# Kernel tuning notes

Measured on AMD Instinct MI355X. Metric: run time of the kernel, lower is better.

The kernel has to match this reference:

```python
import jax, jax.numpy as jnp
import numpy as np

NEG_SLOPE = 0.2

def gat_conv(x, src, dst, W, a_src, a_dst, bias, N):
    # PyG GATConv, heads=1: h = xW; e_ij = LeakyReLU(a_src.h_j + a_dst.h_i)
    h = x @ W                                   # [N, H]
    as_ = h @ a_src                             # [N]
    ad_ = h @ a_dst                             # [N]
    e = jax.nn.leaky_relu(as_[src] + ad_[dst], NEG_SLOPE)   # [E]
    m = jax.ops.segment_max(e, dst, num_segments=N)          # per-target max
    w = jnp.exp(e - m[dst])
    denom = jax.ops.segment_sum(w, dst, num_segments=N)
    alpha = w / (denom[dst] + 1e-16)                          # [E]
    out = jax.ops.segment_sum(alpha[:, None] * h[src], dst, num_segments=N)
    return out + bias


def setup_inputs() -> dict:
    key = jax.random.key(0)
    N, E, D, H, A = 20000, 320000, 256, 256, 8
    ks = jax.random.split(key, 16)
    s = lambda k, shp, fan: jax.random.normal(k, shp, jnp.float32) * (1.0 / np.sqrt(fan))
    return {
        "obs": jax.random.normal(ks[0], (N, D), jnp.float32),
        "edge_index": jax.random.randint(ks[1], (2, E), 0, N, dtype=jnp.int32),
        "W1": s(ks[2], (D, H), D), "a1_src": s(ks[3], (H,), H), "a1_dst": s(ks[4], (H,), H), "b1": jnp.zeros((H,), jnp.float32),
        "W2": s(ks[5], (H, H), H), "a2_src": s(ks[6], (H,), H), "a2_dst": s(ks[7], (H,), H), "b2": jnp.zeros((H,), jnp.float32),
        "Wm1": s(ks[8], (H, H), H), "bm1": jnp.zeros((H,), jnp.float32),
        "Wm2": s(ks[9], (H, A), H), "bm2": jnp.zeros((A,), jnp.float32),
    }


def reference(obs, edge_index, W1, a1_src, a1_dst, b1, W2, a2_src, a2_dst, b2, Wm1, bm1, Wm2, bm2):
    N = obs.shape[0]
    loops = jnp.arange(N, dtype=edge_index.dtype)
    src = jnp.concatenate([edge_index[0], loops])   # add self-loops (PyG default)
    dst = jnp.concatenate([edge_index[1], loops])
    x = jax.nn.relu(gat_conv(obs, src, dst, W1, a1_src, a1_dst, b1, N))
    x = jax.nn.relu(gat_conv(x,   src, dst, W2, a2_src, a2_dst, b2, N))
    x = jax.nn.relu(x @ Wm1 + bm1)
    return jnp.tanh(x @ Wm2 + bm2)
```

## Files before the change

### kernel.cpp

```cpp
#include <hip/hip_runtime.h>
#include <hip/hip_bf16.h>
#include <math.h>
#include <stdio.h>

typedef __attribute__((ext_vector_type(8))) short short8;
typedef __attribute__((ext_vector_type(4))) float f32x4;
typedef __attribute__((ext_vector_type(4))) unsigned short us4;

__device__ __forceinline__ float us2f(unsigned short u) {
    return __uint_as_float(((unsigned)u) << 16);
}
__device__ __forceinline__ unsigned short f2us_rtn(float f) {
    return (unsigned short)__bfloat16_as_ushort(__float2bfloat16(f));
}

__device__ __forceinline__ void stage8(const unsigned short* Ap, unsigned short* dst) {
    *(short8*)dst = *(const short8*)Ap;
}
__device__ __forceinline__ void stage8(const float* Ap, unsigned short* dst) {
    const float4 a = *(const float4*)Ap;
    const float4 b = *(const float4*)(Ap + 4);
    const float f[8] = {a.x, a.y, a.z, a.w, b.x, b.y, b.z, b.w};
    short8 o;
#pragma unroll
    for (int e = 0; e < 8; e++) o[e] = (short)f2us_rtn(f[e]);
    *(short8*)dst = o;
}

__global__ void prep_all(const float* __restrict__ Wa, const float* __restrict__ Wb,
                         const float* __restrict__ Wc,
                         unsigned short* __restrict__ TA, unsigned short* __restrict__ TB,
                         unsigned short* __restrict__ TC,
                         float* __restrict__ as1, float* __restrict__ ad1,
                         float* __restrict__ as2, float* __restrict__ ad2,
                         int* __restrict__ deg,
                         int K, int Nn, int N) {
    const int tot = K * Nn;
    int idx = blockIdx.x * blockDim.x + threadIdx.x;
    if (idx < 3 * tot) {
        const float* W;
        unsigned short* T;
        if (idx < tot) { W = Wa; T = TA; }
        else if (idx < 2 * tot) { W = Wb; T = TB; idx -= tot; }
        else { W = Wc; T = TC; idx -= 2 * tot; }
        const int n = idx / K, k = idx - n * K;
        T[idx] = f2us_rtn(W[(size_t)k * Nn + n]);
        return;
    }
    idx -= 3 * tot;
    if (idx < 5 * N) {
        if (idx < N) as1[idx] = 0.f;
        else if (idx < 2 * N) ad1[idx - N] = 0.f;
        else if (idx < 3 * N) as2[idx - 2 * N] = 0.f;
        else if (idx < 4 * N) ad2[idx - 3 * N] = 0.f;
        else deg[idx - 4 * N] = 0;
    }
}

#define LP 72
template <typename TA>
__global__ __launch_bounds__(256) void gemm_mfma(const TA* __restrict__ A,
                                                 const unsigned short* __restrict__ Bt,
                                                 const float* __restrict__ avs,
                                                 const float* __restrict__ avd,
                                                 float* __restrict__ as_,
                                                 float* __restrict__ ad_,
                                                 unsigned short* __restrict__ C,
                                                 int M, int Nn, int K) {
    __shared__ unsigned short sA[64 * LP];
    __shared__ unsigned short sB[128 * LP];
    const int tid = threadIdx.x;
    const int wave = tid >> 6, lane = tid & 63;
    const int m16 = lane & 15, quad = lane >> 4;
    const int row0 = blockIdx.x * 64, col0 = blockIdx.y * 128;
    const int wr = (wave >> 1) * 32, wc = (wave & 1) * 64;
    const int ar = tid >> 2, akc = (tid & 3) * 8;
    const int bkc = (tid & 7) * 8, bcb = tid >> 3;

    f32x4 acc[2][4] = {};
    for (int k0 = 0; k0 < K; k0 += 64) {
        {
            const int gr = (row0 + ar) < M ? (row0 + ar) : (M - 1);
            const TA* Ap = A + (size_t)gr * K + k0 + akc;
            stage8(Ap,      &sA[ar * LP + akc]);
            stage8(Ap + 32, &sA[ar * LP + akc + 32]);
        }
#pragma unroll
        for (int q = 0; q < 4; q++) {
            const int colq = bcb + 32 * q;
            *(short8*)&sB[colq * LP + bkc] =
                *(const short8*)(Bt + (size_t)(col0 + colq) * K + k0 + bkc);
        }
        __syncthreads();
#pragma unroll
        for (int ks = 0; ks < 2; ks++) {
            short8 ah[2];
#pragma unroll
            for (int mi = 0; mi < 2; mi++)
                ah[mi] = *(const short8*)&sA[(wr + mi * 16 + m16) * LP + ks * 32 + quad * 8];
#pragma unroll
            for (int ni = 0; ni < 4; ni++) {
                const short8 bv = *(const short8*)&sB[(wc + ni * 16 + m16) * LP + ks * 32 + quad * 8];
#pragma unroll
                for (int mi = 0; mi < 2; mi++)
                    acc[mi][ni] = __builtin_amdgcn_mfma_f32_16x16x32_bf16(ah[mi], bv, acc[mi][ni], 0, 0, 0);
            }
        }
        __syncthreads();
    }
    float ps[2][4] = {}, pd[2][4] = {};
#pragma unroll
    for (int mi = 0; mi < 2; mi++) {
        const int orow_base = row0 + wr + mi * 16 + quad * 4;
#pragma unroll
        for (int ni = 0; ni < 4; ni++) {
            const int ocol = col0 + wc + ni * 16 + m16;
            const float asv = avs[ocol], adv = avd[ocol];
#pragma unroll
            for (int r = 0; r < 4; r++) {
                const int orow = orow_base + r;
                if (orow < M) {
                    const float v = acc[mi][ni][r];
                    C[(size_t)orow * Nn + ocol] = f2us_rtn(v);
                    ps[mi][r] = fmaf(v, asv, ps[mi][r]);
                    pd[mi][r] = fmaf(v, adv, pd[mi][r]);
                }
            }
        }
    }
#pragma unroll
    for (int mi = 0; mi < 2; mi++)
#pragma unroll
        for (int r = 0; r < 4; r++)
#pragma unroll
            for (int off = 1; off < 16; off <<= 1) {
                ps[mi][r] += __shfl_xor(ps[mi][r], off);
                pd[mi][r] += __shfl_xor(pd[mi][r], off);
            }
    if (m16 == 0) {
#pragma unroll
        for (int mi = 0; mi < 2; mi++) {
            const int orow_base = row0 + wr + mi * 16 + quad * 4;
#pragma unroll
            for (int r = 0; r < 4; r++) {
                const int orow = orow_base + r;
                if (orow < M) {
                    atomicAdd(&as_[orow], ps[mi][r]);
                    atomicAdd(&ad_[orow], pd[mi][r]);
                }
            }
        }
    }
}

__global__ __launch_bounds__(256) void gemm_head(const unsigned short* __restrict__ A,
                                                 const unsigned short* __restrict__ Bt,
                                                 const float* __restrict__ bias1,
                                                 const float* __restrict__ W2,
                                                 const float* __restrict__ bias2,
                                                 float* __restrict__ out,
                                                 int M, int K, int Aout) {
    __shared__ unsigned short sA[64 * LP];
    __shared__ unsigned short sB[256 * LP];
    __shared__ float pLDS[2][64][8];
    const int tid = threadIdx.x;
    const int wave = tid >> 6, lane = tid & 63;
    const int m16 = lane & 15, quad = lane >> 4;
    const int row0 = blockIdx.x * 64;
    const int wr = (wave >> 1) * 32, wc = (wave & 1) * 128;
    const int ar = tid >> 2, akc = (tid & 3) * 8;
    const int bkc = (tid & 7) * 8, bcb = tid >> 3;

    f32x4 acc[2][8] = {};
    for (int k0 = 0; k0 < K; k0 += 64) {
        {
            const int gr = (row0 + ar) < M ? (row0 + ar) : (M - 1);
            const unsigned short* Ap = A + (size_t)gr * K + k0 + akc;
            *(short8*)&sA[ar * LP + akc]      = *(const short8*)Ap;
            *(short8*)&sA[ar * LP + akc + 32] = *(const short8*)(Ap + 32);
        }
#pragma unroll
        for (int q = 0; q < 8; q++) {
            const int colq = bcb + 32 * q;
            *(short8*)&sB[colq * LP + bkc] =
                *(const short8*)(Bt + (size_t)colq * K + k0 + bkc);
        }
        __syncthreads();
#pragma unroll
        for (int ks = 0; ks < 2; ks++) {
            short8 ah[2];
#pragma unroll
            for (int mi = 0; mi < 2; mi++)
                ah[mi] = *(const short8*)&sA[(wr + mi * 16 + m16) * LP + ks * 32 + quad * 8];
#pragma unroll
            for (int ni = 0; ni < 8; ni++) {
                const short8 bv = *(const short8*)&sB[(wc + ni * 16 + m16) * LP + ks * 32 + quad * 8];
#pragma unroll
                for (int mi = 0; mi < 2; mi++)
                    acc[mi][ni] = __builtin_amdgcn_mfma_f32_16x16x32_bf16(ah[mi], bv, acc[mi][ni], 0, 0, 0);
            }
        }
        __syncthreads();
    }
    float p[2][4][8] = {};
#pragma unroll
    for (int ni = 0; ni < 8; ni++) {
        const int ocol = wc + ni * 16 + m16;
        const float b1v = bias1[ocol];
        float w2[8];
#pragma unroll
        for (int a = 0; a < 8; a++) w2[a] = W2[ocol * 8 + a];
#pragma unroll
        for (int mi = 0; mi < 2; mi++)
#pragma unroll
            for (int r = 0; r < 4; r++) {
                const float v = fmaxf(acc[mi][ni][r] + b1v, 0.f);
#pragma unroll
                for (int a = 0; a < 8; a++) p[mi][r][a] = fmaf(v, w2[a], p[mi][r][a]);
            }
    }
#pragma unroll
    for (int off = 1; off < 16; off <<= 1)
#pragma unroll
        for (int mi = 0; mi < 2; mi++)
#pragma unroll
            for (int r = 0; r < 4; r++)
#pragma unroll
                for (int a = 0; a < 8; a++) p[mi][r][a] += __shfl_xor(p[mi][r][a], off);
    if (m16 == 0) {
        const int half = wc >> 7;
#pragma unroll
        for (int mi = 0; mi < 2; mi++) {
            const int lrow = wr + mi * 16 + quad * 4;
#pragma unroll
            for (int r = 0; r < 4; r++)
#pragma unroll
                for (int a = 0; a < 8; a++) pLDS[half][lrow + r][a] = p[mi][r][a];
        }
    }
    __syncthreads();
#pragma unroll
    for (int u = 0; u < 2; u++) {
        const int idx = tid * 2 + u;
        const int lrow = idx >> 3, a = idx & 7;
        const int orow = row0 + lrow;
        if (orow < M && a < Aout)
            out[(size_t)orow * Aout + a] =
                tanhf(pLDS[0][lrow][a] + pLDS[1][lrow][a] + bias2[a]);
    }
}
#undef LP

__global__ void count_kernel(const int* __restrict__ dstA, int* __restrict__ deg, int E, int Etot) {
    const int e = blockIdx.x * blockDim.x + threadIdx.x;
    if (e >= Etot) return;
    const int d = (e < E) ? dstA[e] : (e - E);
    atomicAdd(&deg[d], 1);
}

__global__ __launch_bounds__(1024) void scan_kernel(const int* __restrict__ deg,
                                                    int* __restrict__ offs,
                                                    int* __restrict__ cursor, int N) {
    __shared__ int sums[1024];
    const int t = threadIdx.x;
    const int chunk = (N + 1023) / 1024;
    const int start = t * chunk;
    int s = 0;
    for (int i = 0; i < chunk; i++) {
        const int p = start + i;
        if (p < N) s += deg[p];
    }
    sums[t] = s;
    __syncthreads();
    for (int off = 1; off < 1024; off <<= 1) {
        const int add = (t >= off) ? sums[t - off] : 0;
        __syncthreads();
        sums[t] += add;
        __syncthreads();
    }
    int run = (t > 0) ? sums[t - 1] : 0;
    for (int i = 0; i < chunk; i++) {
        const int p = start + i;
        if (p < N) { offs[p] = run; cursor[p] = run; run += deg[p]; }
    }
    if (t == 0) offs[N] = sums[1023];
}

__global__ void scatter_kernel(const int* __restrict__ srcA, const int* __restrict__ dstA,
                               int* __restrict__ cursor, int* __restrict__ esrc, int E, int Etot) {
    const int e = blockIdx.x * blockDim.x + threadIdx.x;
    if (e >= Etot) return;
    int s, d;
    if (e < E) { s = srcA[e]; d = dstA[e]; } else { s = d = e - E; }
    const int slot = atomicAdd(&cursor[d], 1);
    esrc[slot] = s;
}

__global__ __launch_bounds__(256) void agg_kernel(const unsigned short* __restrict__ hb,
                                                  const int* __restrict__ offs,
                                                  const int* __restrict__ esrc,
                                                  const float* __restrict__ as_,
                                                  const float* __restrict__ ad_,
                                                  const float* __restrict__ bias,
                                                  unsigned short* __restrict__ xout, int N) {
    const int n = __builtin_amdgcn_readfirstlane(blockIdx.x * 4 + (threadIdx.x >> 6));
    if (n >= N) return;
    const int lane = threadIdx.x & 63;
    const int f0 = lane * 4;
    const int b = offs[n], e2 = offs[n + 1];
    const float adn = ad_[n];
    float a0 = 0.f, a1 = 0.f, a2 = 0.f, a3 = 0.f, wsum = 0.f;
    for (int c0 = b; c0 < e2; c0 += 16) {
        int s = 0;
        float w = 0.f;
        if (lane < 16) {
            const int j = c0 + lane;
            const int jj = j < e2 ? j : e2 - 1;
            s = esrc[jj];
            if (j < e2) {
                float v = as_[s] + adn;
                v = v > 0.f ? v : 0.2f * v;
                w = __expf(v);
                wsum += w;
            }
        }
        int sb[16];
        float wb[16];
#pragma unroll
        for (int u = 0; u < 16; u++) {
            sb[u] = __shfl(s, u);
            wb[u] = __shfl(w, u);
        }
        us4 pv[16];
#pragma unroll
        for (int u = 0; u < 16; u++)
            pv[u] = *(const us4*)(hb + (unsigned)((sb[u] << 8) + f0));
#pragma unroll
        for (int u = 0; u < 16; u++) {
            a0 = fmaf(wb[u], us2f(pv[u][0]), a0);
            a1 = fmaf(wb[u], us2f(pv[u][1]), a1);
            a2 = fmaf(wb[u], us2f(pv[u][2]), a2);
            a3 = fmaf(wb[u], us2f(pv[u][3]), a3);
        }
    }
#pragma unroll
    for (int off = 32; off; off >>= 1) wsum += __shfl_xor(wsum, off);
    const float inv = 1.0f / (wsum + 1e-16f);
    us4 o;
    o[0] = f2us_rtn(fmaxf(a0 * inv + bias[f0], 0.f));
    o[1] = f2us_rtn(fmaxf(a1 * inv + bias[f0 + 1], 0.f));
    o[2] = f2us_rtn(fmaxf(a2 * inv + bias[f0 + 2], 0.f));
    o[3] = f2us_rtn(fmaxf(a3 * inv + bias[f0 + 3], 0.f));
    *(us4*)(xout + (unsigned)((n << 8) + f0)) = o;
}

extern "C" void kernel_launch(void* const* d_in, const int* in_sizes, int n_in,
                              void* d_out, int out_size, void* d_ws, size_t ws_size,
                              hipStream_t stream) {
    const float* obs = (const float*)d_in[0];
    const int* eidx  = (const int*)d_in[1];
    const float* W1  = (const float*)d_in[2];
    const float* a1s = (const float*)d_in[3];
    const float* a1d = (const float*)d_in[4];
    const float* b1  = (const float*)d_in[5];
    const float* W2  = (const float*)d_in[6];
    const float* a2s = (const float*)d_in[7];
    const float* a2d = (const float*)d_in[8];
    const float* b2v = (const float*)d_in[9];
    const float* Wm1 = (const float*)d_in[10];
    const float* bm1 = (const float*)d_in[11];
    const float* Wm2 = (const float*)d_in[12];
    const float* bm2 = (const float*)d_in[13];
    float* out = (float*)d_out;

    const int Hh = in_sizes[3];
    const int Dd = in_sizes[2] / Hh;
    const int N  = in_sizes[0] / Dd;
    const int E  = in_sizes[1] / 2;
    const int Etot = E + N;
    const int Aout = in_sizes[12] / Hh;

    const int* srcA = eidx;
    const int* dstA = eidx + E;

    size_t off = 0;
    char* ws = (char*)d_ws;
    auto alloc = [&](size_t bytes) -> char* {
        char* p = ws + off;
        off = (off + bytes + 15) & ~(size_t)15;
        return p;
    };
    unsigned short* h  = (unsigned short*)alloc((size_t)N * Hh * 2);
    unsigned short* xb = (unsigned short*)alloc((size_t)N * Hh * 2);
    float* as1   = (float*)alloc((size_t)N * 4);
    float* ad1   = (float*)alloc((size_t)N * 4);
    float* as2   = (float*)alloc((size_t)N * 4);
    float* ad2   = (float*)alloc((size_t)N * 4);
    int* deg     = (int*)alloc((size_t)N * 4);
    int* offs    = (int*)alloc((size_t)(N + 1) * 4);
    int* cursor  = (int*)alloc((size_t)N * 4);
    int* esrc    = (int*)alloc((size_t)Etot * 4);
    const size_t wsz = (size_t)Dd * Hh;
    unsigned short* W1t = (unsigned short*)alloc(wsz * 2);
    unsigned short* W2t = (unsigned short*)alloc(wsz * 2);
    unsigned short* Wmt = (unsigned short*)alloc(wsz * 2);

    const int eb = 256;
    const int eg = (Etot + eb - 1) / eb;
    const dim3 ggrid((N + 63) / 64, Hh / 128);
    const int nrow = (N + 63) / 64;
    const int nb4 = (N + 3) / 4;

    const int ptot = 3 * (int)wsz + 5 * N;
    prep_all<<<(ptot + 255) / 256, 256, 0, stream>>>(
        W1, W2, Wm1, W1t, W2t, Wmt, as1, ad1, as2, ad2, deg, Dd, Hh, N);

    count_kernel<<<eg, eb, 0, stream>>>(dstA, deg, E, Etot);
    scan_kernel<<<1, 1024, 0, stream>>>(deg, offs, cursor, N);
    scatter_kernel<<<eg, eb, 0, stream>>>(srcA, dstA, cursor, esrc, E, Etot);

    gemm_mfma<float><<<ggrid, 256, 0, stream>>>(obs, W1t, a1s, a1d, as1, ad1, h, N, Hh, Dd);
    agg_kernel<<<nb4, 256, 0, stream>>>(h, offs, esrc, as1, ad1, b1, xb, N);

    gemm_mfma<unsigned short><<<ggrid, 256, 0, stream>>>(xb, W2t, a2s, a2d, as2, ad2, h, N, Hh, Hh);
    agg_kernel<<<nb4, 256, 0, stream>>>(h, offs, esrc, as2, ad2, b2v, xb, N);

    gemm_head<<<nrow, 256, 0, stream>>>(xb, Wmt, bm1, Wm2, bm2, out, N, Hh, Aout);
}
```

Measured before the change: 265.6 us.

## Prefetch GEMM tiles into registers, pre-convert obs to bf16, widen aggregation loads

Both GEMM kernels now load the next K-tile from global memory into registers while MFMAs run on the current LDS tile, then store it to LDS after a barrier. This is meant to hide global load latency behind compute. The fp32 obs input is converted to bf16 once inside prep_all, so the first GEMM reads bf16 like the second, at the cost of an extra full pass over obs. The aggregation kernel has each half-wave handle alternate edges with 8-wide bf16 loads and combines the two halves with a cross-lane shuffle, halving the gather instructions per edge but adding a reduction step.

```diff
diff --git a/kernel.cpp b/kernel.cpp
--- a/kernel.cpp
+++ b/kernel.cpp
@@ -6,6 +6,7 @@
 typedef __attribute__((ext_vector_type(8))) short short8;
 typedef __attribute__((ext_vector_type(4))) float f32x4;
 typedef __attribute__((ext_vector_type(4))) unsigned short us4;
+typedef __attribute__((ext_vector_type(8))) unsigned short us8;
 
 __device__ __forceinline__ float us2f(unsigned short u) {
     return __uint_as_float(((unsigned)u) << 16);
@@ -14,27 +15,14 @@
     return (unsigned short)__bfloat16_as_ushort(__float2bfloat16(f));
 }
 
-__device__ __forceinline__ void stage8(const unsigned short* Ap, unsigned short* dst) {
-    *(short8*)dst = *(const short8*)Ap;
-}
-__device__ __forceinline__ void stage8(const float* Ap, unsigned short* dst) {
-    const float4 a = *(const float4*)Ap;
-    const float4 b = *(const float4*)(Ap + 4);
-    const float f[8] = {a.x, a.y, a.z, a.w, b.x, b.y, b.z, b.w};
-    short8 o;
-#pragma unroll
-    for (int e = 0; e < 8; e++) o[e] = (short)f2us_rtn(f[e]);
-    *(short8*)dst = o;
-}
-
 __global__ void prep_all(const float* __restrict__ Wa, const float* __restrict__ Wb,
-                         const float* __restrict__ Wc,
+                         const float* __restrict__ Wc, const float* __restrict__ obs,
                          unsigned short* __restrict__ TA, unsigned short* __restrict__ TB,
-                         unsigned short* __restrict__ TC,
+                         unsigned short* __restrict__ TC, unsigned short* __restrict__ obsb,
                          float* __restrict__ as1, float* __restrict__ ad1,
                          float* __restrict__ as2, float* __restrict__ ad2,
                          int* __restrict__ deg,
-                         int K, int Nn, int N) {
+                         int K, int Nn, int N, int nObs8) {
     const int tot = K * Nn;
     int idx = blockIdx.x * blockDim.x + threadIdx.x;
     if (idx < 3 * tot) {
@@ -54,12 +42,22 @@
         else if (idx < 3 * N) as2[idx - 2 * N] = 0.f;
         else if (idx < 4 * N) ad2[idx - 3 * N] = 0.f;
         else deg[idx - 4 * N] = 0;
+        return;
+    }
+    idx -= 5 * N;
+    if (idx < nObs8) {
+        const float4 a = *(const float4*)(obs + (size_t)idx * 8);
+        const float4 b = *(const float4*)(obs + (size_t)idx * 8 + 4);
+        const float f[8] = {a.x, a.y, a.z, a.w, b.x, b.y, b.z, b.w};
+        short8 o;
+#pragma unroll
+        for (int e = 0; e < 8; e++) o[e] = (short)f2us_rtn(f[e]);
+        *(short8*)(obsb + (size_t)idx * 8) = o;
     }
 }
 
 #define LP 72
-template <typename TA>
-__global__ __launch_bounds__(256) void gemm_mfma(const TA* __restrict__ A,
+__global__ __launch_bounds__(256) void gemm_mfma(const unsigned short* __restrict__ A,
                                                  const unsigned short* __restrict__ Bt,
                                                  const float* __restrict__ avs,
                                                  const float* __restrict__ avd,
@@ -76,22 +74,35 @@
     const int wr = (wave >> 1) * 32, wc = (wave & 1) * 64;
     const int ar = tid >> 2, akc = (tid & 3) * 8;
     const int bkc = (tid & 7) * 8, bcb = tid >> 3;
+    const int gr = (row0 + ar) < M ? (row0 + ar) : (M - 1);
+    const unsigned short* Arow = A + (size_t)gr * K + akc;
+    const unsigned short* Bcol = Bt + (size_t)(col0 + bcb) * K + bkc;
+
+    short8 rA0, rA1, rb0, rb1, rb2, rb3;
+    auto LOADT = [&](int k0) {
+        rA0 = *(const short8*)(Arow + k0);
+        rA1 = *(const short8*)(Arow + k0 + 32);
+        rb0 = *(const short8*)(Bcol + k0);
+        rb1 = *(const short8*)(Bcol + (size_t)32 * K + k0);
+        rb2 = *(const short8*)(Bcol + (size_t)64 * K + k0);
+        rb3 = *(const short8*)(Bcol + (size_t)96 * K + k0);
+    };
+    auto STORET = [&]() {
+        *(short8*)&sA[ar * LP + akc]      = rA0;
+        *(short8*)&sA[ar * LP + akc + 32] = rA1;
+        *(short8*)&sB[bcb * LP + bkc]        = rb0;
+        *(short8*)&sB[(bcb + 32) * LP + bkc] = rb1;
+        *(short8*)&sB[(bcb + 64) * LP + bkc] = rb2;
+        *(short8*)&sB[(bcb + 96) * LP + bkc] = rb3;
+    };
 
     f32x4 acc[2][4] = {};
+    LOADT(0);
+    STORET();
+    __syncthreads();
     for (int k0 = 0; k0 < K; k0 += 64) {
-        {
-            const int gr = (row0 + ar) < M ? (row0 + ar) : (M - 1);
-            const TA* Ap = A + (size_t)gr * K + k0 + akc;
-            stage8(Ap,      &sA[ar * LP + akc]);
-            stage8(Ap + 32, &sA[ar * LP + akc + 32]);
-        }
-#pragma unroll
-        for (int q = 0; q < 4; q++) {
-            const int colq = bcb + 32 * q;
-            *(short8*)&sB[colq * LP + bkc] =
-                *(const short8*)(Bt + (size_t)(col0 + colq) * K + k0 + bkc);
-        }
-        __syncthreads();
+        const bool more = (k0 + 64) < K;
+        if (more) LOADT(k0 + 64);
 #pragma unroll
         for (int ks = 0; ks < 2; ks++) {
             short8 ah[2];
@@ -107,6 +118,7 @@
             }
         }
         __syncthreads();
+        if (more) { STORET(); __syncthreads(); }
     }
     float ps[2][4] = {}, pd[2][4] = {};
 #pragma unroll
@@ -170,22 +182,33 @@
     const int wr = (wave >> 1) * 32, wc = (wave & 1) * 128;
     const int ar = tid >> 2, akc = (tid & 3) * 8;
     const int bkc = (tid & 7) * 8, bcb = tid >> 3;
+    const int gr = (row0 + ar) < M ? (row0 + ar) : (M - 1);
+    const unsigned short* Arow = A + (size_t)gr * K + akc;
+    const unsigned short* Bcol = Bt + (size_t)bcb * K + bkc;
+
+    short8 rA0, rA1, rb[8];
+    auto LOADT = [&](int k0) {
+        rA0 = *(const short8*)(Arow + k0);
+        rA1 = *(const short8*)(Arow + k0 + 32);
+#pragma unroll
+        for (int q = 0; q < 8; q++)
+            rb[q] = *(const short8*)(Bcol + (size_t)(32 * q) * K + k0);
+    };
+    auto STORET = [&]() {
+        *(short8*)&sA[ar * LP + akc]      = rA0;
+        *(short8*)&sA[ar * LP + akc + 32] = rA1;
+#pragma unroll
+        for (int q = 0; q < 8; q++)
+            *(short8*)&sB[(bcb + 32 * q) * LP + bkc] = rb[q];
+    };
 
     f32x4 acc[2][8] = {};
+    LOADT(0);
+    STORET();
+    __syncthreads();
     for (int k0 = 0; k0 < K; k0 += 64) {
-        {
-            const int gr = (row0 + ar) < M ? (row0 + ar) : (M - 1);
-            const unsigned short* Ap = A + (size_t)gr * K + k0 + akc;
-            *(short8*)&sA[ar * LP + akc]      = *(const short8*)Ap;
-            *(short8*)&sA[ar * LP + akc + 32] = *(const short8*)(Ap + 32);
-        }
-#pragma unroll
-        for (int q = 0; q < 8; q++) {
-            const int colq = bcb + 32 * q;
-            *(short8*)&sB[colq * LP + bkc] =
-                *(const short8*)(Bt + (size_t)colq * K + k0 + bkc);
-        }
-        __syncthreads();
+        const bool more = (k0 + 64) < K;
+        if (more) LOADT(k0 + 64);
 #pragma unroll
         for (int ks = 0; ks < 2; ks++) {
             short8 ah[2];
@@ -201,6 +224,7 @@
             }
         }
         __syncthreads();
+        if (more) { STORET(); __syncthreads(); }
     }
     float p[2][4][8] = {};
 #pragma unroll
@@ -306,10 +330,12 @@
     const int n = __builtin_amdgcn_readfirstlane(blockIdx.x * 4 + (threadIdx.x >> 6));
     if (n >= N) return;
     const int lane = threadIdx.x & 63;
-    const int f0 = lane * 4;
+    const int half = lane >> 5;
+    const int f0 = (lane & 31) * 8;
     const int b = offs[n], e2 = offs[n + 1];
     const float adn = ad_[n];
-    float a0 = 0.f, a1 = 0.f, a2 = 0.f, a3 = 0.f, wsum = 0.f;
+    float a[8] = {};
+    float wsum = 0.f;
     for (int c0 = b; c0 < e2; c0 += 16) {
         int s = 0;
         float w = 0.f;
@@ -324,34 +350,36 @@
                 wsum += w;
             }
         }
-        int sb[16];
-        float wb[16];
-#pragma unroll
-        for (int u = 0; u < 16; u++) {
-            sb[u] = __shfl(s, u);
-            wb[u] = __shfl(w, u);
-        }
-        us4 pv[16];
-#pragma unroll
-        for (int u = 0; u < 16; u++)
-            pv[u] = *(const us4*)(hb + (unsigned)((sb[u] << 8) + f0));
-#pragma unroll
-        for (int u = 0; u < 16; u++) {
-            a0 = fmaf(wb[u], us2f(pv[u][0]), a0);
-            a1 = fmaf(wb[u], us2f(pv[u][1]), a1);
-            a2 = fmaf(wb[u], us2f(pv[u][2]), a2);
-            a3 = fmaf(wb[u], us2f(pv[u][3]), a3);
-        }
-    }
+        us8 pv[8];
+        float wb[8];
+#pragma unroll
+        for (int u = 0; u < 8; u++) {
+            const int el = 2 * u + half;
+            const int su = __shfl(s, el);
+            wb[u] = __shfl(w, el);
+            pv[u] = *(const us8*)(hb + (unsigned)((su << 8) + f0));
+        }
+#pragma unroll
+        for (int u = 0; u < 8; u++)
+#pragma unroll
+            for (int j2 = 0; j2 < 8; j2++)
+                a[j2] = fmaf(wb[u], us2f(pv[u][j2]), a[j2]);
+    }
+#pragma unroll
+    for (int j2 = 0; j2 < 8; j2++) a[j2] += __shfl_xor(a[j2], 32);
 #pragma unroll
     for (int off = 32; off; off >>= 1) wsum += __shfl_xor(wsum, off);
     const float inv = 1.0f / (wsum + 1e-16f);
-    us4 o;
-    o[0] = f2us_rtn(fmaxf(a0 * inv + bias[f0], 0.f));
-    o[1] = f2us_rtn(fmaxf(a1 * inv + bias[f0 + 1], 0.f));
-    o[2] = f2us_rtn(fmaxf(a2 * inv + bias[f0 + 2], 0.f));
-    o[3] = f2us_rtn(fmaxf(a3 * inv + bias[f0 + 3], 0.f));
-    *(us4*)(xout + (unsigned)((n << 8) + f0)) = o;
+    if (half == 0) {
+        const float4 b0 = *(const float4*)(bias + f0);
+        const float4 b1 = *(const float4*)(bias + f0 + 4);
+        const float bb[8] = {b0.x, b0.y, b0.z, b0.w, b1.x, b1.y, b1.z, b1.w};
+        us8 o;
+#pragma unroll
+        for (int j2 = 0; j2 < 8; j2++)
+            o[j2] = f2us_rtn(fmaxf(a[j2] * inv + bb[j2], 0.f));
+        *(us8*)(xout + (unsigned)((n << 8) + f0)) = o;
+    }
 }
 
 extern "C" void kernel_launch(void* const* d_in, const int* in_sizes, int n_in,
@@ -390,8 +418,9 @@
         off = (off + bytes + 15) & ~(size_t)15;
         return p;
     };
-    unsigned short* h  = (unsigned short*)alloc((size_t)N * Hh * 2);
-    unsigned short* xb = (unsigned short*)alloc((size_t)N * Hh * 2);
+    unsigned short* h    = (unsigned short*)alloc((size_t)N * Hh * 2);
+    unsigned short* xb   = (unsigned short*)alloc((size_t)N * Hh * 2);
+    unsigned short* obsb = (unsigned short*)alloc((size_t)N * Dd * 2);
     float* as1   = (float*)alloc((size_t)N * 4);
     float* ad1   = (float*)alloc((size_t)N * 4);
     float* as2   = (float*)alloc((size_t)N * 4);
@@ -410,19 +439,20 @@
     const dim3 ggrid((N + 63) / 64, Hh / 128);
     const int nrow = (N + 63) / 64;
     const int nb4 = (N + 3) / 4;
-
-    const int ptot = 3 * (int)wsz + 5 * N;
+    const int nObs8 = N * Dd / 8;
+
+    const int ptot = 3 * (int)wsz + 5 * N + nObs8;
     prep_all<<<(ptot + 255) / 256, 256, 0, stream>>>(
-        W1, W2, Wm1, W1t, W2t, Wmt, as1, ad1, as2, ad2, deg, Dd, Hh, N);
+        W1, W2, Wm1, obs, W1t, W2t, Wmt, obsb, as1, ad1, as2, ad2, deg, Dd, Hh, N, nObs8);
 
     count_kernel<<<eg, eb, 0, stream>>>(dstA, deg, E, Etot);
     scan_kernel<<<1, 1024, 0, stream>>>(deg, offs, cursor, N);
     scatter_kernel<<<eg, eb, 0, stream>>>(srcA, dstA, cursor, esrc, E, Etot);
 
-    gemm_mfma<float><<<ggrid, 256, 0, stream>>>(obs, W1t, a1s, a1d, as1, ad1, h, N, Hh, Dd);
+    gemm_mfma<<<ggrid, 256, 0, stream>>>(obsb, W1t, a1s, a1d, as1, ad1, h, N, Hh, Dd);
     agg_kernel<<<nb4, 256, 0, stream>>>(h, offs, esrc, as1, ad1, b1, xb, N);
 
-    gemm_mfma<unsigned short><<<ggrid, 256, 0, stream>>>(xb, W2t, a2s, a2d, as2, ad2, h, N, Hh, Hh);
+    gemm_mfma<<<ggrid, 256, 0, stream>>>(xb, W2t, a2s, a2d, as2, ad2, h, N, Hh, Hh);
     agg_kernel<<<nb4, 256, 0, stream>>>(h, offs, esrc, as2, ad2, b2v, xb, N);
 
     gemm_head<<<nrow, 256, 0, stream>>>(xb, Wmt, bm1, Wm2, bm2, out, N, Hh, Aout);
```

Measured after the change: 261.7 us. About the same (-1.5%).
